# Kernel optimization log

Measured on AMD Instinct MI355X. Metric: run time of the kernel, lower is better.

The kernel has to match this reference:

```python
import jax, jax.numpy as jnp
import numpy as np

B, L, D, P = 8, 2048, 1024, 4  # batch, length, word_dim, phrase_len


def setup_inputs() -> dict:
    key = jax.random.key(0)
    kx, kw, kb = jax.random.split(key, 3)
    x = jax.random.normal(kx, (B, L, D), dtype=jnp.float32)
    # torch nn.Linear(phrase_dim, word_dim): W [out=D, in=D*P], b [D]
    scale = 1.0 / np.sqrt(D * P)
    W = jax.random.uniform(kw, (D, D * P), dtype=jnp.float32, minval=-scale, maxval=scale)
    b = jax.random.uniform(kb, (D,), dtype=jnp.float32, minval=-scale, maxval=scale)
    return {"x": x, "W": W, "b": b}


def reference(x, W, b):
    Bs, Ls, Ds = x.shape
    Ps = W.shape[1] // Ds  # phrase_len
    # gram[i][:, t] = x[:, t - i] (zero for t < i): left-pad by i, keep first L steps.
    # Stack on the LAST axis then reshape, matching torch's contiguous view over
    # (dim, phrase_len) -> feature index d*P + i.
    grams = jnp.stack(
        [jnp.pad(x, ((0, 0), (i, 0), (0, 0)))[:, :Ls, :] for i in range(Ps)],
        axis=-1,
    )  # [B, L, D, P]
    feat = grams.reshape(Bs, Ls, Ds * Ps)  # [B, L, D*P]
    # nn.Linear: y = feat @ W.T + b
    return jnp.einsum("blf,df->bld", feat, W) + b
```

## Files before the change

kernel.cpp:

```cpp
#include <hip/hip_runtime.h>
#include <hip/hip_bf16.h>
#include <stdint.h>

#define Bq 8
#define Lq 2048
#define Dq 1024
#define Pq 4
#define Kq 4096
#define LPAD 2056
#define BM 256
#define BN 128
#define BK 32

typedef __attribute__((ext_vector_type(8))) short short8;
typedef __attribute__((ext_vector_type(4))) float f32x4;

__device__ __forceinline__ unsigned short f2bf(float f) {
  unsigned u = __float_as_uint(f);
  u += 0x7FFFu + ((u >> 16) & 1u);
  return (unsigned short)(u >> 16);
}

__device__ __forceinline__ void gload_lds16(const void* g, void* l) {
  __builtin_amdgcn_global_load_lds(
      (const __attribute__((address_space(1))) void*)g,
      (__attribute__((address_space(3))) void*)l, 16, 0, 0);
}

__global__ void k_prep(const float* __restrict__ x, const float* __restrict__ W,
                       unsigned short* __restrict__ xp, unsigned short* __restrict__ Wp) {
  if (blockIdx.x < 8224u) {
    unsigned g = blockIdx.x * blockDim.x + threadIdx.x;
    unsigned base = g * 8;
    const unsigned total = (unsigned)Bq * LPAD * Dq;
    if (base >= total) return;
    unsigned t = base >> 10;
    unsigned b = t / LPAD;
    unsigned r = t - b * LPAD;
    unsigned d = base & 1023;
    short8 o;
    if (r >= 3 && r < 3 + Lq) {
      const float* s = x + ((size_t)b * Lq + (r - 3)) * Dq + d;
      float4 v0 = *(const float4*)(s);
      float4 v1 = *(const float4*)(s + 4);
      o[0] = (short)f2bf(v0.x); o[1] = (short)f2bf(v0.y);
      o[2] = (short)f2bf(v0.z); o[3] = (short)f2bf(v0.w);
      o[4] = (short)f2bf(v1.x); o[5] = (short)f2bf(v1.y);
      o[6] = (short)f2bf(v1.z); o[7] = (short)f2bf(v1.w);
    } else {
      o = (short8)0;
    }
    *(short8*)(xp + base) = o;
  } else {
    unsigned g = (blockIdx.x - 8224u) * blockDim.x + threadIdx.x;
    unsigned base = g * 8;
    unsigned d = base >> 12;
    unsigned rem = base & 4095;
    unsigned dp = rem >> 2;
    const float4* src = (const float4*)(W + base);
    float4 v0 = src[0];
    float4 v1 = src[1];
    float a0[4] = {v0.x, v0.y, v0.z, v0.w};
    float a1[4] = {v1.x, v1.y, v1.z, v1.w};
#pragma unroll
    for (int i = 0; i < 4; ++i) {
      unsigned packed = (unsigned)f2bf(a0[i]) | ((unsigned)f2bf(a1[i]) << 16);
      *(unsigned*)(Wp + (size_t)d * 4096 + (size_t)i * 1024 + dp) = packed;
    }
  }
}


#define VM6 asm volatile("s_waitcnt vmcnt(6)" ::: "memory")
#define VM0 asm volatile("s_waitcnt vmcnt(0)" ::: "memory")
#define BAR __builtin_amdgcn_s_barrier()

#define STAGE_AB(AIMM, BIMM, kt) do { \
    const unsigned sclA_ = (((unsigned)(bRow0 - ((kt) >> 5))) << 11) + (((unsigned)(kt) & 31u) << 6); \
    const unsigned sclB_ = nScl + ((unsigned)(kt) << 6); \
    _Pragma("unroll") for (int j_ = 0; j_ < 4; ++j_) \
      gload_lds16((const char*)xp + (thrA + (unsigned)(j_ * 131072) + sclA_), \
                  lds + (AIMM) + (j_ << 12) + (tid << 4)); \
    _Pragma("unroll") for (int j_ = 0; j_ < 2; ++j_) \
      gload_lds16((const char*)Wp + (thrB + (unsigned)(j_ * 524288) + sclB_), \
                  lds + (BIMM) + (j_ << 12) + (tid << 4)); \
  } while (0)

#define READS(AIMM, BIMM) do { \
    _Pragma("unroll") for (int mi_ = 0; mi_ < 8; ++mi_) \
      fa[mi_] = *(const short8*)(lds + aVG[mi_] + (AIMM)); \
    _Pragma("unroll") for (int ni_ = 0; ni_ < 4; ++ni_) \
      fb[ni_] = *(const short8*)(lds + bVG[ni_] + (BIMM)); \
  } while (0)

#define MFMA32 do { \
    __builtin_amdgcn_s_setprio(1); \
    _Pragma("unroll") for (int mi_ = 0; mi_ < 8; ++mi_) \
    _Pragma("unroll") for (int ni_ = 0; ni_ < 4; ++ni_) \
      acc[mi_][ni_] = __builtin_amdgcn_mfma_f32_16x16x32_bf16( \
          fa[mi_], fb[ni_], acc[mi_][ni_], 0, 0, 0); \
    __builtin_amdgcn_s_setprio(0); \
  } while (0)

#define PHASE(AR, BR, AS, BS, kt) do { \
    READS(AR, BR); STAGE_AB(AS, BS, kt); MFMA32; VM6; BAR; \
  } while (0)

__global__ void __launch_bounds__(256, 2)
k_gemm(const unsigned short* __restrict__ xp,
       const unsigned short* __restrict__ Wp,
       const float* __restrict__ bias,
       float* __restrict__ out) {
  __shared__ __attribute__((aligned(16))) unsigned char lds[73728];

  const int tid  = threadIdx.x;
  const int lane = tid & 63;
  const int w    = tid >> 6;
  const int wm   = w >> 1;
  const int wn   = w & 1;

  const int bid = blockIdx.x;
  const int swz = (bid & 7) * 64 + (bid >> 3);
  const int m0 = (swz >> 3) * BM;
  const int n0 = (swz & 7) * BN;
  const int b  = m0 >> 11;
  const int l0 = m0 & 2047;
  const int bRow0 = b * LPAD + l0 + 3;
  const unsigned nScl = (unsigned)n0 << 13;

  const unsigned rS   = (unsigned)(tid >> 2);
  const unsigned clS  = (unsigned)((tid & 3) ^ ((tid >> 3) & 3));
  const unsigned thrA = (rS << 11) + (clS << 4);
  const unsigned thrB = (rS << 13) + (clS << 4);

  const int r4 = lane & 15;
  const int chunk = ((lane >> 4) ^ ((r4 >> 1) & 3)) << 4;
  unsigned aVG[8], bVG[4];
#pragma unroll
  for (int mi = 0; mi < 8; ++mi)
    aVG[mi] = (unsigned)(((wm * 128 + mi * 16 + r4) << 6) + chunk);
#pragma unroll
  for (int ni = 0; ni < 4; ++ni)
    bVG[ni] = (unsigned)(((wn * 64 + ni * 16 + r4) << 6) + chunk);

  f32x4 acc[8][4] = {};
  short8 fa[8], fb[4];

  STAGE_AB(24576, 0, 0);
  STAGE_AB(40960, 8192, 1);
  VM6;
  BAR;

#pragma unroll 1
  for (int it = 0; it < 42; ++it) {
    const int k0 = it * 3;
    PHASE(24576, 0,     57344, 16384, k0 + 2);
    PHASE(40960, 8192,  24576, 0,     k0 + 3);
    PHASE(57344, 16384, 40960, 8192,  k0 + 4);
  }

  READS(24576, 0);
  MFMA32;
  VM0; BAR;
  READS(40960, 8192);
  MFMA32;

#pragma unroll
  for (int ni = 0; ni < 4; ++ni) {
    const int col = n0 + wn * 64 + ni * 16 + r4;
    const float bv = bias[col];
#pragma unroll
    for (int mi = 0; mi < 8; ++mi) {
      const int row0 = m0 + wm * 128 + mi * 16 + ((lane >> 4) << 2);
#pragma unroll
      for (int t2 = 0; t2 < 4; ++t2)
        out[(size_t)(row0 + t2) * Dq + col] = acc[mi][ni][t2] + bv;
    }
  }
}

__global__ void k_naive(const float* __restrict__ x, const float* __restrict__ W,
                        const float* __restrict__ bias, float* __restrict__ out) {
  size_t g = (size_t)blockIdx.x * blockDim.x + threadIdx.x;
  const size_t total = (size_t)Bq * Lq * Dq;
  if (g >= total) return;
  int d = (int)(g & 1023);
  int l = (int)((g >> 10) & 2047);
  int b = (int)(g >> 21);
  float s = bias[d];
  for (int i = 0; i < Pq; ++i) {
    if (l - i < 0) continue;
    const float* xr = x + ((size_t)b * Lq + (l - i)) * Dq;
    const float* wr = W + (size_t)d * Kq + i;
    float accv = 0.f;
    for (int dp = 0; dp < Dq; ++dp) accv += xr[dp] * wr[(size_t)dp * 4];
    s += accv;
  }
  out[g] = s;
}

extern "C" void kernel_launch(void* const* d_in, const int* in_sizes, int n_in,
                              void* d_out, int out_size, void* d_ws, size_t ws_size,
                              hipStream_t stream) {
  const float* x    = (const float*)d_in[0];
  const float* W    = (const float*)d_in[1];
  const float* bias = (const float*)d_in[2];
  float* out = (float*)d_out;

  const size_t WP_BYTES = (size_t)Dq * Kq * sizeof(unsigned short);
  const size_t XP_BYTES = (size_t)Bq * LPAD * Dq * sizeof(unsigned short);

  if (ws_size < WP_BYTES + XP_BYTES) {
    const size_t total = (size_t)Bq * Lq * Dq;
    k_naive<<<(unsigned)((total + 255) / 256), 256, 0, stream>>>(x, W, bias, out);
    return;
  }

  unsigned short* Wp = (unsigned short*)d_ws;
  unsigned short* xp = (unsigned short*)((char*)d_ws + WP_BYTES);

  k_prep<<<10272, 256, 0, stream>>>(x, W, xp, Wp);
  k_gemm<<<dim3((Bq * Lq / BM) * (Dq / BN)), 256, 0, stream>>>(xp, Wp, bias, out);
}
```

Baseline: 152.0 us.

## Enlarge GEMM tile to 256x256 with 8 waves and direct-register B fragments

Doubles the output tile to 256x256 with 512 threads and a BK of 64. The weight matrix is pre-laid out in MFMA fragment order so each wave loads its B operand straight from global into registers, and only A is staged through LDS in double-buffered half-tiles. This aims to raise arithmetic intensity per block, cut LDS traffic for B and reduce barrier count per K step. It gives up B reuse through LDS across waves, since the waves sharing a column tile each read the same B from global/L2, and it raises register pressure.

```diff
diff --git a/kernel.cpp b/kernel.cpp
--- a/kernel.cpp
+++ b/kernel.cpp
@@ -9,8 +9,8 @@
 #define Kq 4096
 #define LPAD 2056
 #define BM 256
-#define BN 128
-#define BK 32
+#define BN 256
+#define BK 64
 
 typedef __attribute__((ext_vector_type(8))) short short8;
 typedef __attribute__((ext_vector_type(4))) float f32x4;
@@ -28,7 +28,7 @@
 }
 
 __global__ void k_prep(const float* __restrict__ x, const float* __restrict__ W,
-                       unsigned short* __restrict__ xp, unsigned short* __restrict__ Wp) {
+                       unsigned short* __restrict__ xp, unsigned short* __restrict__ Wf) {
   if (blockIdx.x < 8224u) {
     unsigned g = blockIdx.x * blockDim.x + threadIdx.x;
     unsigned base = g * 8;
@@ -53,128 +53,146 @@
     *(short8*)(xp + base) = o;
   } else {
     unsigned g = (blockIdx.x - 8224u) * blockDim.x + threadIdx.x;
-    unsigned base = g * 8;
-    unsigned d = base >> 12;
-    unsigned rem = base & 4095;
-    unsigned dp = rem >> 2;
-    const float4* src = (const float4*)(W + base);
-    float4 v0 = src[0];
-    float4 v1 = src[1];
-    float a0[4] = {v0.x, v0.y, v0.z, v0.w};
-    float a1[4] = {v1.x, v1.y, v1.z, v1.w};
-#pragma unroll
-    for (int i = 0; i < 4; ++i) {
-      unsigned packed = (unsigned)f2bf(a0[i]) | ((unsigned)f2bf(a1[i]) << 16);
-      *(unsigned*)(Wp + (size_t)d * 4096 + (size_t)i * 1024 + dp) = packed;
-    }
-  }
-}
-
-
-#define VM6 asm volatile("s_waitcnt vmcnt(6)" ::: "memory")
+    unsigned d  = g >> 9;
+    unsigned kc = g & 511;
+    unsigned i  = kc >> 7;
+    unsigned dp0 = (kc & 127) << 3;
+    const float* src = W + (size_t)d * 4096 + (size_t)dp0 * 4 + i;
+    short8 o;
+#pragma unroll
+    for (int e = 0; e < 8; ++e) o[e] = (short)f2bf(src[e * 4]);
+    unsigned kt = kc >> 3;
+    unsigned kk = (kc >> 2) & 1;
+    unsigned ni = (d >> 4) & 3;
+    unsigned lane = (d & 15) + ((kc & 3) << 4);
+    unsigned a16 = ((((d >> 6) * 64 + kt) * 8) + kk * 4 + ni) * 64 + lane;
+    *(short8*)(Wf + ((size_t)a16 << 3)) = o;
+  }
+}
+
+
+#define VM2 asm volatile("s_waitcnt vmcnt(2)" ::: "memory")
 #define VM0 asm volatile("s_waitcnt vmcnt(0)" ::: "memory")
 #define BAR __builtin_amdgcn_s_barrier()
 
-#define STAGE_AB(AIMM, BIMM, kt) do { \
-    const unsigned sclA_ = (((unsigned)(bRow0 - ((kt) >> 5))) << 11) + (((unsigned)(kt) & 31u) << 6); \
-    const unsigned sclB_ = nScl + ((unsigned)(kt) << 6); \
-    _Pragma("unroll") for (int j_ = 0; j_ < 4; ++j_) \
-      gload_lds16((const char*)xp + (thrA + (unsigned)(j_ * 131072) + sclA_), \
-                  lds + (AIMM) + (j_ << 12) + (tid << 4)); \
-    _Pragma("unroll") for (int j_ = 0; j_ < 2; ++j_) \
-      gload_lds16((const char*)Wp + (thrB + (unsigned)(j_ * 524288) + sclB_), \
-                  lds + (BIMM) + (j_ << 12) + (tid << 4)); \
+#define LOAD_B(kt) do { \
+    const unsigned short* wb_ = Wf + (((unsigned)(nIdx64 + (kt))) << 12); \
+    _Pragma("unroll") for (int s_ = 0; s_ < 8; ++s_) \
+      bF[s_ & 3][s_ >> 2] = *(const short8*)(wb_ + (s_ << 9) + lan8); \
   } while (0)
 
-#define READS(AIMM, BIMM) do { \
-    _Pragma("unroll") for (int mi_ = 0; mi_ < 8; ++mi_) \
-      fa[mi_] = *(const short8*)(lds + aVG[mi_] + (AIMM)); \
+#define STAGE_H(buf, kt, h) do { \
+    const unsigned sclA_ = (((unsigned)(bRow0 - ((kt) >> 4))) << 11) + (((unsigned)(kt) & 15u) << 7); \
+    _Pragma("unroll") for (int q_ = 0; q_ < 2; ++q_) { \
+      const int qq_ = (h) * 2 + q_; \
+      gload_lds16((const char*)xp + (thrA + (unsigned)(qq_ << 17) + sclA_), \
+                  lds + ((buf) << 15) + (qq_ << 13) + (tid << 4)); \
+    } } while (0)
+
+#define RD_A(buf, h) do { \
+    _Pragma("unroll") for (int mi_ = 0; mi_ < 4; ++mi_) \
+    _Pragma("unroll") for (int kk_ = 0; kk_ < 2; ++kk_) \
+      fa[mi_][kk_] = *(const short8*)(lds + (((buf) << 15) + ((h) << 13)) + aRC[mi_][kk_]); \
+  } while (0)
+
+#define MFMAQ(mh) do { \
+    __builtin_amdgcn_s_setprio(1); \
+    _Pragma("unroll") for (int kk_ = 0; kk_ < 2; ++kk_) \
+    _Pragma("unroll") for (int mi_ = 0; mi_ < 4; ++mi_) \
     _Pragma("unroll") for (int ni_ = 0; ni_ < 4; ++ni_) \
-      fb[ni_] = *(const short8*)(lds + bVG[ni_] + (BIMM)); \
-  } while (0)
-
-#define MFMA32 do { \
-    __builtin_amdgcn_s_setprio(1); \
-    _Pragma("unroll") for (int mi_ = 0; mi_ < 8; ++mi_) \
-    _Pragma("unroll") for (int ni_ = 0; ni_ < 4; ++ni_) \
-      acc[mi_][ni_] = __builtin_amdgcn_mfma_f32_16x16x32_bf16( \
-          fa[mi_], fb[ni_], acc[mi_][ni_], 0, 0, 0); \
+      acc[(mh) * 4 + mi_][ni_] = __builtin_amdgcn_mfma_f32_16x16x32_bf16( \
+          fa[mi_][kk_], bF[ni_][kk_], acc[(mh) * 4 + mi_][ni_], 0, 0, 0); \
     __builtin_amdgcn_s_setprio(0); \
   } while (0)
 
-#define PHASE(AR, BR, AS, BS, kt) do { \
-    READS(AR, BR); STAGE_AB(AS, BS, kt); MFMA32; VM6; BAR; \
-  } while (0)
-
-__global__ void __launch_bounds__(256, 2)
+__global__ void __launch_bounds__(512, 2)
 k_gemm(const unsigned short* __restrict__ xp,
-       const unsigned short* __restrict__ Wp,
+       const unsigned short* __restrict__ Wf,
        const float* __restrict__ bias,
        float* __restrict__ out) {
-  __shared__ __attribute__((aligned(16))) unsigned char lds[73728];
+  __shared__ __attribute__((aligned(16))) unsigned char lds[65536];
 
   const int tid  = threadIdx.x;
   const int lane = tid & 63;
   const int w    = tid >> 6;
-  const int wm   = w >> 1;
-  const int wn   = w & 1;
+  const int wm   = w >> 2;
+  const int wn   = w & 3;
 
   const int bid = blockIdx.x;
-  const int swz = (bid & 7) * 64 + (bid >> 3);
-  const int m0 = (swz >> 3) * BM;
-  const int n0 = (swz & 7) * BN;
+  const int swz = (bid & 7) * 32 + (bid >> 3);
+  const int m0 = (swz >> 2) * BM;
+  const int n0 = (swz & 3) * BN;
   const int b  = m0 >> 11;
   const int l0 = m0 & 2047;
   const int bRow0 = b * LPAD + l0 + 3;
-  const unsigned nScl = (unsigned)n0 << 13;
-
-  const unsigned rS   = (unsigned)(tid >> 2);
-  const unsigned clS  = (unsigned)((tid & 3) ^ ((tid >> 3) & 3));
-  const unsigned thrA = (rS << 11) + (clS << 4);
-  const unsigned thrB = (rS << 13) + (clS << 4);
-
-  const int r4 = lane & 15;
-  const int chunk = ((lane >> 4) ^ ((r4 >> 1) & 3)) << 4;
-  unsigned aVG[8], bVG[4];
-#pragma unroll
-  for (int mi = 0; mi < 8; ++mi)
-    aVG[mi] = (unsigned)(((wm * 128 + mi * 16 + r4) << 6) + chunk);
-#pragma unroll
-  for (int ni = 0; ni < 4; ++ni)
-    bVG[ni] = (unsigned)(((wn * 64 + ni * 16 + r4) << 6) + chunk);
+  const unsigned nIdx64 = (unsigned)(((n0 >> 6) + wn)) << 6;
+  const unsigned lan8 = (unsigned)lane << 3;
+
+  const unsigned srow = (unsigned)(tid >> 3);
+  const unsigned clog = ((unsigned)((tid & 7) ^ ((tid >> 3) & 7)));
+  const unsigned thrA = (srow << 11) + (clog << 4);
+
+  unsigned aRC[4][2];
+  {
+#pragma unroll
+    for (int mi = 0; mi < 4; ++mi)
+#pragma unroll
+      for (int kk = 0; kk < 2; ++kk) {
+        const int cb = (kk * 64 + ((lane >> 4) << 4)) ^ ((lane & 7) << 4);
+        aRC[mi][kk] = (unsigned)((wm << 14) + ((mi * 16 + (lane & 15)) << 7) + cb);
+      }
+  }
 
   f32x4 acc[8][4] = {};
-  short8 fa[8], fb[4];
-
-  STAGE_AB(24576, 0, 0);
-  STAGE_AB(40960, 8192, 1);
-  VM6;
+  short8 fa[4][2], bF[4][2];
+
+  STAGE_H(0, 0, 0);
+  STAGE_H(0, 0, 1);
+  STAGE_H(1, 1, 0);
+  VM2;
   BAR;
 
 #pragma unroll 1
-  for (int it = 0; it < 42; ++it) {
-    const int k0 = it * 3;
-    PHASE(24576, 0,     57344, 16384, k0 + 2);
-    PHASE(40960, 8192,  24576, 0,     k0 + 3);
-    PHASE(57344, 16384, 40960, 8192,  k0 + 4);
-  }
-
-  READS(24576, 0);
-  MFMA32;
-  VM0; BAR;
-  READS(40960, 8192);
-  MFMA32;
-
-#pragma unroll
-  for (int ni = 0; ni < 4; ++ni) {
-    const int col = n0 + wn * 64 + ni * 16 + r4;
+  for (int it = 0; it < 31; ++it) {
+    const int T = it * 2;
+    LOAD_B(T);
+    STAGE_H(1, T + 1, 1);
+    RD_A(0, 0);
+    VM2; MFMAQ(0); BAR;
+    STAGE_H(0, T + 2, 0);
+    RD_A(0, 1);
+    MFMAQ(1); BAR;
+    LOAD_B(T + 1);
+    STAGE_H(0, T + 2, 1);
+    RD_A(1, 0);
+    VM2; MFMAQ(0); BAR;
+    STAGE_H(1, T + 3, 0);
+    RD_A(1, 1);
+    MFMAQ(1); BAR;
+  }
+
+  LOAD_B(62);
+  STAGE_H(1, 63, 1);
+  RD_A(0, 0);
+  VM2; MFMAQ(0); BAR;
+  RD_A(0, 1);
+  MFMAQ(1); BAR;
+  LOAD_B(63);
+  RD_A(1, 0);
+  VM0; MFMAQ(0); BAR;
+  RD_A(1, 1);
+  MFMAQ(1);
+
+#pragma unroll
+  for (int nig = 0; nig < 4; ++nig) {
+    const int col = n0 + wn * 64 + nig * 16 + (lane & 15);
     const float bv = bias[col];
 #pragma unroll
-    for (int mi = 0; mi < 8; ++mi) {
-      const int row0 = m0 + wm * 128 + mi * 16 + ((lane >> 4) << 2);
+    for (int mig = 0; mig < 8; ++mig) {
+      const int row0 = m0 + wm * 128 + mig * 16 + ((lane >> 4) << 2);
 #pragma unroll
       for (int t2 = 0; t2 < 4; ++t2)
-        out[(size_t)(row0 + t2) * Dq + col] = acc[mi][ni][t2] + bv;
+        out[(size_t)(row0 + t2) * Dq + col] = acc[mig][nig][t2] + bv;
     }
   }
 }
@@ -207,18 +225,18 @@
   const float* bias = (const float*)d_in[2];
   float* out = (float*)d_out;
 
-  const size_t WP_BYTES = (size_t)Dq * Kq * sizeof(unsigned short);
+  const size_t WF_BYTES = (size_t)Dq * Kq * sizeof(unsigned short);
   const size_t XP_BYTES = (size_t)Bq * LPAD * Dq * sizeof(unsigned short);
 
-  if (ws_size < WP_BYTES + XP_BYTES) {
+  if (ws_size < WF_BYTES + XP_BYTES) {
     const size_t total = (size_t)Bq * Lq * Dq;
     k_naive<<<(unsigned)((total + 255) / 256), 256, 0, stream>>>(x, W, bias, out);
     return;
   }
 
-  unsigned short* Wp = (unsigned short*)d_ws;
-  unsigned short* xp = (unsigned short*)((char*)d_ws + WP_BYTES);
-
-  k_prep<<<10272, 256, 0, stream>>>(x, W, xp, Wp);
-  k_gemm<<<dim3((Bq * Lq / BM) * (Dq / BN)), 256, 0, stream>>>(xp, Wp, bias, out);
-}
+  unsigned short* Wf = (unsigned short*)d_ws;
+  unsigned short* xp = (unsigned short*)((char*)d_ws + WF_BYTES);
+
+  k_prep<<<10272, 256, 0, stream>>>(x, W, xp, Wf);
+  k_gemm<<<dim3((Bq * Lq / BM) * (Dq / BN)), 512, 0, stream>>>(xp, Wf, bias, out);
+}
```

Result: slower. 161.8 us (+6.4%).
